# Optimization experiments

Hardware: AMD Instinct MI355X
Metric: run time of the kernel (lower is better)

## Reference

```python
import jax, jax.numpy as jnp
import numpy as np

D, H, FF, EPS = 1024, 16, 4096, 1e-5

def _ln(x, g, b):
    m = jnp.mean(x, axis=-1, keepdims=True)
    v = jnp.var(x, axis=-1, keepdims=True)
    return (x - m) * jax.lax.rsqrt(v + EPS) * g + b

def setup_inputs() -> dict:
    key = jax.random.key(0)
    ks = jax.random.split(key, 8)
    b, t = 2, 2048
    return {
        "x": jax.random.normal(ks[0], (b, t, D), jnp.float32),
        "prev_attn": jax.random.normal(ks[1], (b, H, t, t), jnp.float32) * 0.1,
        "w_qkv": jax.random.normal(ks[2], (D, 3 * D), jnp.float32) * (D ** -0.5),
        "w_out": jax.random.normal(ks[3], (D, D), jnp.float32) * (D ** -0.5),
        "w1": jax.random.normal(ks[4], (D, FF), jnp.float32) * (D ** -0.5),
        "b1": jnp.zeros((FF,), jnp.float32),
        "w2": jax.random.normal(ks[5], (FF, D), jnp.float32) * (FF ** -0.5),
        "b2": jnp.zeros((D,), jnp.float32),
        "g1": jnp.ones((D,), jnp.float32),
        "be1": jnp.zeros((D,), jnp.float32),
        "g2": jnp.ones((D,), jnp.float32),
        "be2": jnp.zeros((D,), jnp.float32),
    }

def reference(x, prev_attn, w_qkv, w_out, w1, b1, w2, b2, g1, be1, g2, be2):
    b, t, d = x.shape
    h, hd = H, d // H
    scale = hd ** -0.5
    qkv = _ln(x, g1, be1) @ w_qkv                       # [b,t,3d]
    q, k, v = jnp.split(qkv, 3, axis=-1)
    q, k, v = [z.reshape(b, t, h, hd).transpose(0, 2, 1, 3) for z in (q, k, v)]
    attn = jnp.einsum('bhid,bhjd->bhij', q, k) * scale + prev_attn
    attn = jax.nn.softmax(attn, axis=-1)                # [b,h,t,t]
    out = jnp.einsum('bhij,bhjd->bhid', attn, v).transpose(0, 2, 1, 3).reshape(b, t, d)
    x = x + out @ w_out
    hdn = _ln(x, g2, be2)
    ffn = jax.nn.gelu(hdn @ w1 + b1, approximate=False) @ w2 + b2
    x = x + ffn
    return (x, jax.lax.stop_gradient(attn))
```

## Files before the change

### kernel.cpp

```cpp
#include <hip/hip_runtime.h>
#include <hip/hip_bf16.h>
#include <math.h>

#define T_SEQ 2048
#define D_MODEL 1024
#define N_HEADS 16
#define HD 64
#define FF_DIM 4096
#define N_ROWS 4096
#define LDQKV 3072

typedef __bf16 bf16x8 __attribute__((ext_vector_type(8)));
typedef float f32x4 __attribute__((ext_vector_type(4)));

__device__ __forceinline__ unsigned short f2bf(float f) {
  union { float f; unsigned u; } v; v.f = f;
  unsigned r = v.u + 0x7FFFu + ((v.u >> 16) & 1u);
  return (unsigned short)(r >> 16);
}
__device__ __forceinline__ float bf2f(unsigned short u) {
  union { unsigned u; float f; } v; v.u = ((unsigned)u) << 16;
  return v.f;
}

__device__ __forceinline__ void gld_lds16(const void* g, void* l) {
  __builtin_amdgcn_global_load_lds(
      (const __attribute__((address_space(1))) unsigned int*)g,
      (__attribute__((address_space(3))) unsigned int*)l, 16, 0, 0);
}

__global__ __launch_bounds__(256) void transpose_w(const float* __restrict__ src,
                                                   unsigned short* __restrict__ dst,
                                                   int R, int C) {
  __shared__ float tile[32][33];
  int c0 = blockIdx.x * 32, r0 = blockIdx.y * 32;
  int tx = threadIdx.x & 31, ty = threadIdx.x >> 5;
#pragma unroll
  for (int i = 0; i < 32; i += 8)
    tile[ty + i][tx] = src[(size_t)(r0 + ty + i) * C + c0 + tx];
  __syncthreads();
#pragma unroll
  for (int i = 0; i < 32; i += 8)
    dst[(size_t)(c0 + ty + i) * R + r0 + tx] = f2bf(tile[tx][ty + i]);
}

__global__ __launch_bounds__(256) void ln_kernel(const float* __restrict__ x,
                                                 const float* __restrict__ g,
                                                 const float* __restrict__ be,
                                                 unsigned short* __restrict__ out) {
  int row = blockIdx.x;
  float4 v = ((const float4*)(x + (size_t)row * D_MODEL))[threadIdx.x];
  float s = v.x + v.y + v.z + v.w;
  float ss = v.x * v.x + v.y * v.y + v.z * v.z + v.w * v.w;
#pragma unroll
  for (int o = 32; o; o >>= 1) { s += __shfl_down(s, o); ss += __shfl_down(ss, o); }
  __shared__ float red[8];
  int wid = threadIdx.x >> 6, lane = threadIdx.x & 63;
  if (lane == 0) { red[wid] = s; red[4 + wid] = ss; }
  __syncthreads();
  if (threadIdx.x == 0) {
    float S0 = red[0] + red[1] + red[2] + red[3];
    float S1 = red[4] + red[5] + red[6] + red[7];
    float m = S0 * (1.0f / D_MODEL);
    red[0] = m;
    red[1] = rsqrtf(S1 * (1.0f / D_MODEL) - m * m + 1e-5f);
  }
  __syncthreads();
  float m = red[0], inv = red[1];
  float4 gv = ((const float4*)g)[threadIdx.x];
  float4 bv = ((const float4*)be)[threadIdx.x];
  ushort4 o;
  o.x = f2bf((v.x - m) * inv * gv.x + bv.x);
  o.y = f2bf((v.y - m) * inv * gv.y + bv.y);
  o.z = f2bf((v.z - m) * inv * gv.z + bv.z);
  o.w = f2bf((v.w - m) * inv * gv.w + bv.w);
  ((ushort4*)(out + (size_t)row * D_MODEL))[threadIdx.x] = o;
}

template <int EPI>
__global__ __launch_bounds__(256) void gemm_bt(const unsigned short* __restrict__ A,
                                               const unsigned short* __restrict__ Bt,
                                               int M, int N, int K,
                                               void* __restrict__ outp,
                                               const float* __restrict__ bias,
                                               const float* __restrict__ res) {
  __shared__ __align__(16) unsigned short As[2][128 * 32];
  __shared__ __align__(16) unsigned short Bs[2][128 * 32];
  int tid = threadIdx.x;
  int m0 = blockIdx.x * 128, n0 = blockIdx.y * 128;
  int w = tid >> 6, l = tid & 63;
  int wm = w >> 1, wn = w & 1;
  int lr = l & 15, lg = l >> 4;
  f32x4 acc[4][4] = {};
  const unsigned short* ap0 = A + (size_t)(m0 + (tid >> 2)) * K + (tid & 3) * 8;
  const unsigned short* ap1 = ap0 + (size_t)64 * K;
  const unsigned short* bp0 = Bt + (size_t)(n0 + (tid >> 2)) * K + (tid & 3) * 8;
  const unsigned short* bp1 = bp0 + (size_t)64 * K;
  int ldso = (tid & ~63) * 8;
  auto stage = [&](int buf, int k0) {
    gld_lds16(ap0 + k0, &As[buf][ldso]);
    gld_lds16(ap1 + k0, &As[buf][2048 + ldso]);
    gld_lds16(bp0 + k0, &Bs[buf][ldso]);
    gld_lds16(bp1 + k0, &Bs[buf][2048 + ldso]);
  };
  int nt = K >> 5;
  stage(0, 0);
  __syncthreads();
  for (int t = 0; t < nt; t++) {
    int cur = t & 1;
    if (t + 1 < nt) stage(cur ^ 1, (t + 1) * 32);
    bf16x8 af[4], bfr[4];
#pragma unroll
    for (int i = 0; i < 4; i++) {
      af[i] = *(const bf16x8*)(&As[cur][(wm * 64 + i * 16 + lr) * 32 + lg * 8]);
      bfr[i] = *(const bf16x8*)(&Bs[cur][(wn * 64 + i * 16 + lr) * 32 + lg * 8]);
    }
#pragma unroll
    for (int i = 0; i < 4; i++)
#pragma unroll
      for (int j = 0; j < 4; j++)
        acc[i][j] = __builtin_amdgcn_mfma_f32_16x16x32_bf16(af[i], bfr[j], acc[i][j], 0, 0, 0);
    __syncthreads();
  }
#pragma unroll
  for (int i = 0; i < 4; i++) {
#pragma unroll
    for (int j = 0; j < 4; j++) {
      int col = n0 + wn * 64 + j * 16 + lr;
#pragma unroll
      for (int r = 0; r < 4; r++) {
        int row = m0 + wm * 64 + i * 16 + lg * 4 + r;
        size_t idx = (size_t)row * N + col;
        float v = acc[i][j][r];
        if (EPI == 0) {
          if (col < 1024) v *= 0.125f;
          ((unsigned short*)outp)[idx] = f2bf(v);
        } else if (EPI == 2) {
          float t2 = v + bias[col];
          ((unsigned short*)outp)[idx] = f2bf(0.5f * t2 * (1.0f + erff(t2 * 0.70710678f)));
        }
      }
    }
  }
}

template <int EPI>
__global__ __launch_bounds__(256) void gemm_bt2(const unsigned short* __restrict__ A,
                                                const unsigned short* __restrict__ Bt,
                                                int M, int N, int K,
                                                void* __restrict__ outp,
                                                const float* __restrict__ bias,
                                                const float* __restrict__ res) {
  __shared__ __align__(16) unsigned short As[2][64 * 64];
  __shared__ __align__(16) unsigned short Bs[2][128 * 64];
  int tid = threadIdx.x;
  int m0 = blockIdx.x * 64, n0 = blockIdx.y * 128;
  int w = tid >> 6, l = tid & 63;
  int lr = l & 15, lg = l >> 4;
  f32x4 acc[4][2] = {};
  int srow = tid >> 3;
  int scolb = ((tid & 7) * 16) ^ ((srow & 7) << 4);
  const unsigned short* apg = A + (size_t)(m0 + srow) * K + (scolb >> 1);
  const unsigned short* bpg = Bt + (size_t)(n0 + srow) * K + (scolb >> 1);
  auto stage = [&](int buf, int k0) {
    gld_lds16(apg + k0, &As[buf][tid * 8]);
    gld_lds16(apg + (size_t)32 * K + k0, &As[buf][2048 + tid * 8]);
    gld_lds16(bpg + k0, &Bs[buf][tid * 8]);
    gld_lds16(bpg + (size_t)32 * K + k0, &Bs[buf][2048 + tid * 8]);
    gld_lds16(bpg + (size_t)64 * K + k0, &Bs[buf][4096 + tid * 8]);
    gld_lds16(bpg + (size_t)96 * K + k0, &Bs[buf][6144 + tid * 8]);
  };
  int nt = K >> 6;
  stage(0, 0);
  __syncthreads();
  for (int t = 0; t < nt; t++) {
    int cur = t & 1;
    if (t + 1 < nt) stage(cur ^ 1, (t + 1) * 64);
#pragma unroll
    for (int kk = 0; kk < 2; kk++) {
      int cb = (lg * 16 + kk * 64) ^ ((lr & 7) << 4);
      bf16x8 af[4], bfr[2];
#pragma unroll
      for (int i = 0; i < 4; i++)
        af[i] = *(const bf16x8*)((const char*)As[cur] + (i * 16 + lr) * 128 + cb);
#pragma unroll
      for (int j = 0; j < 2; j++)
        bfr[j] = *(const bf16x8*)((const char*)Bs[cur] + (w * 32 + j * 16 + lr) * 128 + cb);
#pragma unroll
      for (int i = 0; i < 4; i++)
#pragma unroll
        for (int j = 0; j < 2; j++)
          acc[i][j] = __builtin_amdgcn_mfma_f32_16x16x32_bf16(af[i], bfr[j], acc[i][j], 0, 0, 0);
    }
    __syncthreads();
  }
#pragma unroll
  for (int i = 0; i < 4; i++) {
#pragma unroll
    for (int j = 0; j < 2; j++) {
      int col = n0 + w * 32 + j * 16 + lr;
#pragma unroll
      for (int r = 0; r < 4; r++) {
        int row = m0 + i * 16 + lg * 4 + r;
        size_t idx = (size_t)row * N + col;
        float v = acc[i][j][r];
        if (EPI == 1) {
          ((float*)outp)[idx] = res[idx] + v;
        } else {
          ((float*)outp)[idx] = v + bias[col] + res[idx];
        }
      }
    }
  }
}

__global__ __launch_bounds__(256) void repack_kv(const unsigned short* __restrict__ qkv,
                                                 unsigned short* __restrict__ kt,
                                                 unsigned short* __restrict__ vt2) {
  __shared__ unsigned short tile[64][66];
  int bh = blockIdx.x >> 5, tt = blockIdx.x & 31;
  int b = bh >> 4, h = bh & 15;
  int t0 = tt * 64;
  int tid = threadIdx.x;
  const unsigned short* ksrc = qkv + (size_t)(b * T_SEQ + t0) * LDQKV + D_MODEL + h * HD;
  unsigned short* kdst = kt + ((size_t)bh * T_SEQ + t0) * HD;
#pragma unroll
  for (int i = 0; i < 16; i++) {
    int e = i * 256 + tid;
    int tr = e >> 6, d = e & 63;
    kdst[(size_t)tr * HD + d] = ksrc[(size_t)tr * LDQKV + d];
  }
  const unsigned short* vsrc = qkv + (size_t)(b * T_SEQ + t0) * LDQKV + 2 * D_MODEL + h * HD;
#pragma unroll
  for (int i = 0; i < 16; i++) {
    int e = i * 256 + tid;
    int tr = e >> 6, d = e & 63;
    tile[tr][d] = vsrc[(size_t)tr * LDQKV + d];
  }
  __syncthreads();
  unsigned short* vdst = vt2 + (size_t)bh * 64 * HD * 32 + (size_t)(t0 >> 5) * HD * 32;
#pragma unroll
  for (int i = 0; i < 16; i++) {
    int e = i * 256 + tid;
    int d = e >> 6, tr = e & 63;
    vdst[(size_t)((tr >> 5) * HD + d) * 32 + (tr & 31)] = tile[tr][d];
  }
}

__global__ __launch_bounds__(512, 4) void attn_kernel(const unsigned short* __restrict__ qkv,
                                                      const unsigned short* __restrict__ kt,
                                                      const unsigned short* __restrict__ vt2,
                                                      const float* __restrict__ prev,
                                                      float* __restrict__ attn_out,
                                                      unsigned short* __restrict__ ctx) {
  __shared__ __align__(16) unsigned short S[16 * 2048];
  int bid = blockIdx.x;
  int nb = (bid & 7) * 512 + (bid >> 3);
  int bh = nb >> 7, rt = nb & 127;
  int b = bh >> 4, h = bh & 15;
  int r0 = rt * 16;
  int tid = threadIdx.x, w = tid >> 6, l = tid & 63;
  int lr = l & 15, lg = l >> 4;

  const unsigned short* qb = qkv + (size_t)(b * T_SEQ + r0 + lr) * LDQKV + h * HD + lg * 8;
  bf16x8 qf0 = *(const bf16x8*)(qb);
  bf16x8 qf1 = *(const bf16x8*)(qb + 32);

  const unsigned short* kb0 = kt + (size_t)bh * T_SEQ * HD + lg * 8;
#pragma unroll
  for (int nt = 0; nt < 16; nt++) {
    int c = w * 256 + nt * 16 + lr;
    const unsigned short* kp = kb0 + (size_t)c * HD;
    bf16x8 kf0 = *(const bf16x8*)(kp);
    bf16x8 kf1 = *(const bf16x8*)(kp + 32);
    f32x4 a = {};
    __builtin_amdgcn_s_setprio(1);
    a = __builtin_amdgcn_mfma_f32_16x16x32_bf16(qf0, kf0, a, 0, 0, 0);
    a = __builtin_amdgcn_mfma_f32_16x16x32_bf16(qf1, kf1, a, 0, 0, 0);
    __builtin_amdgcn_s_setprio(0);
#pragma unroll
    for (int r = 0; r < 4; r++) {
      int row = lg * 4 + r;
      int byteoff = (c * 2) ^ ((row & 7) << 4);
      *(unsigned short*)((char*)S + row * 4096 + byteoff) = f2bf(a[r]);
    }
  }
  __syncthreads();

  const float* pvb = prev + ((size_t)bh * T_SEQ + r0 + 2 * w) * T_SEQ;
  float* arow0 = attn_out + ((size_t)bh * T_SEQ + r0 + 2 * w) * T_SEQ;
#pragma unroll
  for (int rr = 0; rr < 2; rr++) {
    int row = w * 2 + rr;
    char* Sr = (char*)S + row * 4096;
    int xv = (row & 7) << 4;
    const float* pr = pvb + (size_t)rr * T_SEQ;
    float* ar = arow0 + (size_t)rr * T_SEQ;
    f32x4 sv[8];
    float mx = -1e30f;
#pragma unroll
    for (int i = 0; i < 8; i++) {
      int c = l * 4 + i * 256;
      ushort4 sraw = *(const ushort4*)(Sr + ((2 * c) ^ xv));
      f32x4 p = *(const f32x4*)(pr + c);
      sv[i][0] = bf2f(sraw.x) + p[0];
      sv[i][1] = bf2f(sraw.y) + p[1];
      sv[i][2] = bf2f(sraw.z) + p[2];
      sv[i][3] = bf2f(sraw.w) + p[3];
      mx = fmaxf(mx, fmaxf(fmaxf(sv[i][0], sv[i][1]), fmaxf(sv[i][2], sv[i][3])));
    }
#pragma unroll
    for (int o = 32; o; o >>= 1) mx = fmaxf(mx, __shfl_xor(mx, o));
    float sum = 0.f;
#pragma unroll
    for (int i = 0; i < 8; i++) {
      sv[i][0] = __expf(sv[i][0] - mx);
      sv[i][1] = __expf(sv[i][1] - mx);
      sv[i][2] = __expf(sv[i][2] - mx);
      sv[i][3] = __expf(sv[i][3] - mx);
      sum += sv[i][0] + sv[i][1] + sv[i][2] + sv[i][3];
    }
#pragma unroll
    for (int o = 32; o; o >>= 1) sum += __shfl_xor(sum, o);
    float inv = 1.0f / sum;
#pragma unroll
    for (int i = 0; i < 8; i++) {
      int c = l * 4 + i * 256;
      float4 p4;
      p4.x = sv[i][0] * inv; p4.y = sv[i][1] * inv;
      p4.z = sv[i][2] * inv; p4.w = sv[i][3] * inv;
      *(float4*)(ar + c) = p4;
      ushort4 pbf;
      pbf.x = f2bf(p4.x); pbf.y = f2bf(p4.y); pbf.z = f2bf(p4.z); pbf.w = f2bf(p4.w);
      *(ushort4*)(Sr + ((2 * c) ^ xv)) = pbf;
    }
  }
  __syncthreads();

  f32x4 pacc[4] = {};
  const unsigned short* vb = vt2 + (size_t)bh * 64 * HD * 32;
#pragma unroll
  for (int kt_i = 0; kt_i < 8; kt_i++) {
    int kb = w * 256 + kt_i * 32;
    char* Sr = (char*)S + lr * 4096;
    int byteoff = ((kb + lg * 8) * 2) ^ ((lr & 7) << 4);
    bf16x8 af = *(const bf16x8*)(Sr + byteoff);
    const unsigned short* vtile = vb + (size_t)(kb >> 5) * HD * 32;
    __builtin_amdgcn_s_setprio(1);
#pragma unroll
    for (int nj = 0; nj < 4; nj++) {
      const unsigned short* vp = vtile + (size_t)(nj * 16 + lr) * 32 + lg * 8;
      bf16x8 bv = *(const bf16x8*)(vp);
      pacc[nj] = __builtin_amdgcn_mfma_f32_16x16x32_bf16(af, bv, pacc[nj], 0, 0, 0);
    }
    __builtin_amdgcn_s_setprio(0);
  }
  __syncthreads();

  float* P = (float*)S;
#pragma unroll
  for (int nj = 0; nj < 4; nj++)
#pragma unroll
    for (int r = 0; r < 4; r++)
      P[(w * 16 + lg * 4 + r) * 64 + nj * 16 + lr] = pacc[nj][r];
  __syncthreads();
  for (int e = tid; e < 1024; e += 512) {
    float s = 0.f;
#pragma unroll
    for (int ww = 0; ww < 8; ww++) s += P[ww * 1024 + e];
    int row = e >> 6, col = e & 63;
    ctx[(size_t)(b * T_SEQ + r0 + row) * D_MODEL + h * HD + col] = f2bf(s);
  }
}

extern "C" void kernel_launch(void* const* d_in, const int* in_sizes, int n_in,
                              void* d_out, int out_size, void* d_ws, size_t ws_size,
                              hipStream_t stream) {
  const float* x = (const float*)d_in[0];
  const float* prev = (const float*)d_in[1];
  const float* w_qkv = (const float*)d_in[2];
  const float* w_out = (const float*)d_in[3];
  const float* w1 = (const float*)d_in[4];
  const float* b1 = (const float*)d_in[5];
  const float* w2 = (const float*)d_in[6];
  const float* b2 = (const float*)d_in[7];
  const float* g1 = (const float*)d_in[8];
  const float* be1 = (const float*)d_in[9];
  const float* g2 = (const float*)d_in[10];
  const float* be2 = (const float*)d_in[11];
  float* out_x = (float*)d_out;
  float* out_attn = out_x + (size_t)N_ROWS * D_MODEL;

  char* p = (char*)d_ws;
  auto alloc = [&](size_t bytes) -> void* {
    void* r = (void*)p;
    p += (bytes + 255) & ~(size_t)255;
    return r;
  };
  unsigned short* wqkvT = (unsigned short*)alloc((size_t)3072 * 1024 * 2);
  unsigned short* woutT = (unsigned short*)alloc((size_t)1024 * 1024 * 2);
  unsigned short* w1T   = (unsigned short*)alloc((size_t)4096 * 1024 * 2);
  unsigned short* w2T   = (unsigned short*)alloc((size_t)1024 * 4096 * 2);
  unsigned short* ln1b  = (unsigned short*)alloc((size_t)N_ROWS * 1024 * 2);
  unsigned short* qkvb  = (unsigned short*)alloc((size_t)N_ROWS * 3072 * 2);
  unsigned short* ktb   = (unsigned short*)alloc((size_t)32 * 2048 * 64 * 2);
  unsigned short* vt2b  = (unsigned short*)alloc((size_t)32 * 64 * 64 * 32 * 2);
  unsigned short* ctxb  = (unsigned short*)alloc((size_t)N_ROWS * 1024 * 2);
  float*          x2b   = (float*)alloc((size_t)N_ROWS * 1024 * 4);
  unsigned short* ln2b  = (unsigned short*)alloc((size_t)N_ROWS * 1024 * 2);
  unsigned short* hb    = (unsigned short*)alloc((size_t)N_ROWS * 4096 * 2);

  transpose_w<<<dim3(3072 / 32, 1024 / 32), 256, 0, stream>>>(w_qkv, wqkvT, 1024, 3072);
  transpose_w<<<dim3(1024 / 32, 1024 / 32), 256, 0, stream>>>(w_out, woutT, 1024, 1024);
  transpose_w<<<dim3(4096 / 32, 1024 / 32), 256, 0, stream>>>(w1, w1T, 1024, 4096);
  transpose_w<<<dim3(1024 / 32, 4096 / 32), 256, 0, stream>>>(w2, w2T, 4096, 1024);

  ln_kernel<<<N_ROWS, 256, 0, stream>>>(x, g1, be1, ln1b);
  gemm_bt<0><<<dim3(32, 24), 256, 0, stream>>>(ln1b, wqkvT, N_ROWS, 3072, 1024, qkvb, nullptr, nullptr);
  repack_kv<<<32 * 32, 256, 0, stream>>>(qkvb, ktb, vt2b);
  attn_kernel<<<32 * 128, 512, 0, stream>>>(qkvb, ktb, vt2b, prev, out_attn, ctxb);
  gemm_bt2<1><<<dim3(64, 8), 256, 0, stream>>>(ctxb, woutT, N_ROWS, 1024, 1024, x2b, nullptr, x);
  ln_kernel<<<N_ROWS, 256, 0, stream>>>(x2b, g2, be2, ln2b);
  gemm_bt<2><<<dim3(32, 32), 256, 0, stream>>>(ln2b, w1T, N_ROWS, 4096, 1024, hb, b1, nullptr);
  gemm_bt2<3><<<dim3(64, 8), 256, 0, stream>>>(hb, w2T, N_ROWS, 1024, 4096, out_x, b2, x2b);
}
```

Measured before the change: 559.3 us.

## Fuse K/V repack into QKV GEMM epilogue, merge weight transposes, use packed bf16 converts

The QKV GEMM epilogue now writes K and V directly into the head-major layouts the attention kernel reads, so the separate repack_kv kernel and its extra pass over the K/V slice of the QKV buffer are removed. The four weight-transpose launches are merged into one launch that selects its matrix by block index. LayerNorm and the softmax probability store now use the hardware v_cvt_pk_bf16_f32 instruction instead of manual bit-rounding. Risks: the scattered K/V epilogue stores are less coalesced than the old repack writes, and the hardware convert may round slightly differently from the manual routine.

```diff
diff --git a/kernel.cpp b/kernel.cpp
--- a/kernel.cpp
+++ b/kernel.cpp
@@ -22,6 +22,11 @@
   union { unsigned u; float f; } v; v.u = ((unsigned)u) << 16;
   return v.f;
 }
+__device__ __forceinline__ unsigned cvtpk(float a, float b) {
+  unsigned r;
+  asm("v_cvt_pk_bf16_f32 %0, %1, %2" : "=v"(r) : "v"(a), "v"(b));
+  return r;
+}
 
 __device__ __forceinline__ void gld_lds16(const void* g, void* l) {
   __builtin_amdgcn_global_load_lds(
@@ -29,11 +34,22 @@
       (__attribute__((address_space(3))) unsigned int*)l, 16, 0, 0);
 }
 
-__global__ __launch_bounds__(256) void transpose_w(const float* __restrict__ src,
-                                                   unsigned short* __restrict__ dst,
-                                                   int R, int C) {
+__global__ __launch_bounds__(256) void transpose_all(const float* __restrict__ wq,
+                                                     const float* __restrict__ wo,
+                                                     const float* __restrict__ w1,
+                                                     const float* __restrict__ w2,
+                                                     unsigned short* __restrict__ wqT,
+                                                     unsigned short* __restrict__ woT,
+                                                     unsigned short* __restrict__ w1T,
+                                                     unsigned short* __restrict__ w2T) {
+  int bid = blockIdx.x;
+  const float* src; unsigned short* dst; int R, C, bx, by;
+  if (bid < 3072)       { src = wq; dst = wqT; R = 1024; C = 3072; bx = bid % 96;  by = bid / 96; }
+  else if (bid < 4096)  { int t = bid - 3072; src = wo; dst = woT; R = 1024; C = 1024; bx = t % 32;  by = t / 32; }
+  else if (bid < 8192)  { int t = bid - 4096; src = w1; dst = w1T; R = 1024; C = 4096; bx = t % 128; by = t / 128; }
+  else                  { int t = bid - 8192; src = w2; dst = w2T; R = 4096; C = 1024; bx = t % 32;  by = t / 32; }
   __shared__ float tile[32][33];
-  int c0 = blockIdx.x * 32, r0 = blockIdx.y * 32;
+  int c0 = bx * 32, r0 = by * 32;
   int tx = threadIdx.x & 31, ty = threadIdx.x >> 5;
 #pragma unroll
   for (int i = 0; i < 32; i += 8)
@@ -69,12 +85,10 @@
   float m = red[0], inv = red[1];
   float4 gv = ((const float4*)g)[threadIdx.x];
   float4 bv = ((const float4*)be)[threadIdx.x];
-  ushort4 o;
-  o.x = f2bf((v.x - m) * inv * gv.x + bv.x);
-  o.y = f2bf((v.y - m) * inv * gv.y + bv.y);
-  o.z = f2bf((v.z - m) * inv * gv.z + bv.z);
-  o.w = f2bf((v.w - m) * inv * gv.w + bv.w);
-  ((ushort4*)(out + (size_t)row * D_MODEL))[threadIdx.x] = o;
+  uint2 o;
+  o.x = cvtpk((v.x - m) * inv * gv.x + bv.x, (v.y - m) * inv * gv.y + bv.y);
+  o.y = cvtpk((v.z - m) * inv * gv.z + bv.z, (v.w - m) * inv * gv.w + bv.w);
+  ((uint2*)(out + (size_t)row * D_MODEL))[threadIdx.x] = o;
 }
 
 template <int EPI>
@@ -83,7 +97,8 @@
                                                int M, int N, int K,
                                                void* __restrict__ outp,
                                                const float* __restrict__ bias,
-                                               const float* __restrict__ res) {
+                                               unsigned short* __restrict__ ktp,
+                                               unsigned short* __restrict__ vtp) {
   __shared__ __align__(16) unsigned short As[2][128 * 32];
   __shared__ __align__(16) unsigned short Bs[2][128 * 32];
   int tid = threadIdx.x;
@@ -127,17 +142,33 @@
 #pragma unroll
     for (int j = 0; j < 4; j++) {
       int col = n0 + wn * 64 + j * 16 + lr;
-#pragma unroll
-      for (int r = 0; r < 4; r++) {
-        int row = m0 + wm * 64 + i * 16 + lg * 4 + r;
-        size_t idx = (size_t)row * N + col;
-        float v = acc[i][j][r];
-        if (EPI == 0) {
-          if (col < 1024) v *= 0.125f;
-          ((unsigned short*)outp)[idx] = f2bf(v);
-        } else if (EPI == 2) {
-          float t2 = v + bias[col];
-          ((unsigned short*)outp)[idx] = f2bf(0.5f * t2 * (1.0f + erff(t2 * 0.70710678f)));
+      int X = m0 + wm * 64 + i * 16 + lg * 4;
+      if (EPI == 0) {
+        if (col < 1024) {
+#pragma unroll
+          for (int r = 0; r < 4; r++)
+            ((unsigned short*)outp)[(size_t)(X + r) * N + col] = f2bf(acc[i][j][r] * 0.125f);
+        } else if (col < 2048) {
+          int hk = (col - 1024) >> 6, d = col & 63;
+          int bq = X >> 11, tq = X & 2047;
+          unsigned short* kp = ktp + (((size_t)(bq * 16 + hk) << 11) + tq) * HD + d;
+#pragma unroll
+          for (int r = 0; r < 4; r++) kp[(size_t)r * HD] = f2bf(acc[i][j][r]);
+        } else {
+          int hv = (col - 2048) >> 6, d = col & 63;
+          int bq = X >> 11, tq = X & 2047;
+          unsigned short* vp = vtp + ((((size_t)(bq * 16 + hv) * 64 + (tq >> 5)) * HD + d) * 32 + (tq & 31));
+          ushort4 o4;
+          o4.x = f2bf(acc[i][j][0]); o4.y = f2bf(acc[i][j][1]);
+          o4.z = f2bf(acc[i][j][2]); o4.w = f2bf(acc[i][j][3]);
+          *(ushort4*)vp = o4;
+        }
+      } else {
+#pragma unroll
+        for (int r = 0; r < 4; r++) {
+          float t2 = acc[i][j][r] + bias[col];
+          ((unsigned short*)outp)[(size_t)(X + r) * N + col] =
+              f2bf(0.5f * t2 * (1.0f + erff(t2 * 0.70710678f)));
         }
       }
     }
@@ -214,39 +245,6 @@
   }
 }
 
-__global__ __launch_bounds__(256) void repack_kv(const unsigned short* __restrict__ qkv,
-                                                 unsigned short* __restrict__ kt,
-                                                 unsigned short* __restrict__ vt2) {
-  __shared__ unsigned short tile[64][66];
-  int bh = blockIdx.x >> 5, tt = blockIdx.x & 31;
-  int b = bh >> 4, h = bh & 15;
-  int t0 = tt * 64;
-  int tid = threadIdx.x;
-  const unsigned short* ksrc = qkv + (size_t)(b * T_SEQ + t0) * LDQKV + D_MODEL + h * HD;
-  unsigned short* kdst = kt + ((size_t)bh * T_SEQ + t0) * HD;
-#pragma unroll
-  for (int i = 0; i < 16; i++) {
-    int e = i * 256 + tid;
-    int tr = e >> 6, d = e & 63;
-    kdst[(size_t)tr * HD + d] = ksrc[(size_t)tr * LDQKV + d];
-  }
-  const unsigned short* vsrc = qkv + (size_t)(b * T_SEQ + t0) * LDQKV + 2 * D_MODEL + h * HD;
-#pragma unroll
-  for (int i = 0; i < 16; i++) {
-    int e = i * 256 + tid;
-    int tr = e >> 6, d = e & 63;
-    tile[tr][d] = vsrc[(size_t)tr * LDQKV + d];
-  }
-  __syncthreads();
-  unsigned short* vdst = vt2 + (size_t)bh * 64 * HD * 32 + (size_t)(t0 >> 5) * HD * 32;
-#pragma unroll
-  for (int i = 0; i < 16; i++) {
-    int e = i * 256 + tid;
-    int d = e >> 6, tr = e & 63;
-    vdst[(size_t)((tr >> 5) * HD + d) * 32 + (tr & 31)] = tile[tr][d];
-  }
-}
-
 __global__ __launch_bounds__(512, 4) void attn_kernel(const unsigned short* __restrict__ qkv,
                                                       const unsigned short* __restrict__ kt,
                                                       const unsigned short* __restrict__ vt2,
@@ -330,9 +328,10 @@
       p4.x = sv[i][0] * inv; p4.y = sv[i][1] * inv;
       p4.z = sv[i][2] * inv; p4.w = sv[i][3] * inv;
       *(float4*)(ar + c) = p4;
-      ushort4 pbf;
-      pbf.x = f2bf(p4.x); pbf.y = f2bf(p4.y); pbf.z = f2bf(p4.z); pbf.w = f2bf(p4.w);
-      *(ushort4*)(Sr + ((2 * c) ^ xv)) = pbf;
+      uint2 pk;
+      pk.x = cvtpk(p4.x, p4.y);
+      pk.y = cvtpk(p4.z, p4.w);
+      *(uint2*)(Sr + ((2 * c) ^ xv)) = pk;
     }
   }
   __syncthreads();
@@ -410,17 +409,13 @@
   unsigned short* ln2b  = (unsigned short*)alloc((size_t)N_ROWS * 1024 * 2);
   unsigned short* hb    = (unsigned short*)alloc((size_t)N_ROWS * 4096 * 2);
 
-  transpose_w<<<dim3(3072 / 32, 1024 / 32), 256, 0, stream>>>(w_qkv, wqkvT, 1024, 3072);
-  transpose_w<<<dim3(1024 / 32, 1024 / 32), 256, 0, stream>>>(w_out, woutT, 1024, 1024);
-  transpose_w<<<dim3(4096 / 32, 1024 / 32), 256, 0, stream>>>(w1, w1T, 1024, 4096);
-  transpose_w<<<dim3(1024 / 32, 4096 / 32), 256, 0, stream>>>(w2, w2T, 4096, 1024);
+  transpose_all<<<12288, 256, 0, stream>>>(w_qkv, w_out, w1, w2, wqkvT, woutT, w1T, w2T);
 
   ln_kernel<<<N_ROWS, 256, 0, stream>>>(x, g1, be1, ln1b);
-  gemm_bt<0><<<dim3(32, 24), 256, 0, stream>>>(ln1b, wqkvT, N_ROWS, 3072, 1024, qkvb, nullptr, nullptr);
-  repack_kv<<<32 * 32, 256, 0, stream>>>(qkvb, ktb, vt2b);
+  gemm_bt<0><<<dim3(32, 24), 256, 0, stream>>>(ln1b, wqkvT, N_ROWS, 3072, 1024, qkvb, nullptr, ktb, vt2b);
   attn_kernel<<<32 * 128, 512, 0, stream>>>(qkvb, ktb, vt2b, prev, out_attn, ctxb);
   gemm_bt2<1><<<dim3(64, 8), 256, 0, stream>>>(ctxb, woutT, N_ROWS, 1024, 1024, x2b, nullptr, x);
   ln_kernel<<<N_ROWS, 256, 0, stream>>>(x2b, g2, be2, ln2b);
-  gemm_bt<2><<<dim3(32, 32), 256, 0, stream>>>(ln2b, w1T, N_ROWS, 4096, 1024, hb, b1, nullptr);
+  gemm_bt<2><<<dim3(32, 32), 256, 0, stream>>>(ln2b, w1T, N_ROWS, 4096, 1024, hb, b1, nullptr, nullptr);
   gemm_bt2<3><<<dim3(64, 8), 256, 0, stream>>>(hb, w2T, N_ROWS, 1024, 4096, out_x, b2, x2b);
 }
```

Measured after the change: 552.5 us. No clear change (-1.2%).
